# Optimization experiments

Hardware: AMD Instinct MI355X
Metric: run time of the kernel (lower is better)

## Reference

```python
import jax, jax.numpy as jnp
import numpy as np

NUM_HEADS = 16
ROPE_THETA = 10000.0


def setup_inputs() -> dict:
    key = jax.random.key(0)
    ks = jax.random.split(key, 5)
    B, S, D = 4, 2048, 2048
    scale = 0.02
    return {
        "x": jax.random.normal(ks[0], (B, S, D), dtype=jnp.float32),
        "wq": jax.random.normal(ks[1], (D, D), dtype=jnp.float32) * scale,
        "bq": jnp.zeros((D,), dtype=jnp.float32),
        "wk": jax.random.normal(ks[2], (D, D), dtype=jnp.float32) * scale,
        "bk": jnp.zeros((D,), dtype=jnp.float32),
        "wv": jax.random.normal(ks[3], (D, D), dtype=jnp.float32) * scale,
        "bv": jnp.zeros((D,), dtype=jnp.float32),
        "wo": jax.random.normal(ks[4], (D, D), dtype=jnp.float32) * scale,
        "bo": jnp.zeros((D,), dtype=jnp.float32),
    }


def _rotate_half(t):
    t1, t2 = jnp.split(t, 2, axis=-1)
    return jnp.concatenate([-t2, t1], axis=-1)


def _rope_cos_sin(seq_len, head_dim, dtype):
    inv_freq = 1.0 / (ROPE_THETA ** (jnp.arange(0, head_dim, 2, dtype=jnp.float32) / head_dim))
    freqs = jnp.einsum("s,d->sd", jnp.arange(seq_len, dtype=jnp.float32), inv_freq)
    emb = jnp.concatenate([freqs, freqs], axis=-1)  # [S, Dh]
    return jnp.cos(emb).astype(dtype)[None, None], jnp.sin(emb).astype(dtype)[None, None]


def reference(x, wq, bq, wk, bk, wv, bv, wo, bo):
    B, S, D = x.shape
    H = NUM_HEADS
    Dh = D // H

    def proj_heads(w, b):
        # [B,S,D] -> [B,H,S,Dh]
        return (x @ w.T + b).reshape(B, S, H, Dh).transpose(0, 2, 1, 3)

    q = proj_heads(wq, bq)
    k = proj_heads(wk, bk)
    v = proj_heads(wv, bv)

    cos, sin = _rope_cos_sin(S, Dh, x.dtype)
    q = q * cos + _rotate_half(q) * sin
    k = k * cos + _rotate_half(k) * sin

    # non-causal SDPA
    scores = jnp.einsum("bhsd,bhtd->bhst", q, k) / jnp.sqrt(jnp.asarray(Dh, x.dtype))
    attn = jax.nn.softmax(scores, axis=-1)
    ctx = jnp.einsum("bhst,bhtd->bhsd", attn, v)  # [B,H,S,Dh]

    ctx = ctx.transpose(0, 2, 1, 3).reshape(B, S, D)
    return ctx @ wo.T + bo
```

## Files before the change

kernel.cpp:

```cpp
#include <hip/hip_runtime.h>
#include <hip/hip_bf16.h>

typedef __bf16 bf16_t;
typedef __bf16 bf16x8 __attribute__((ext_vector_type(8)));
typedef float f32x4 __attribute__((ext_vector_type(4)));

#define MFMA16(A, B, C) __builtin_amdgcn_mfma_f32_16x16x32_bf16(A, B, C, 0, 0, 0)

#define GLOAD_LDS16(gp, lp)                                           \
    __builtin_amdgcn_global_load_lds(                                 \
        (const __attribute__((address_space(1))) void*)(gp),          \
        (__attribute__((address_space(3))) void*)(lp), 16, 0, 0)

__device__ __forceinline__ uint32_t pack2(bf16_t a, bf16_t b) {
    union { bf16_t h[2]; uint32_t u; } x;
    x.h[0] = a; x.h[1] = b;
    return x.u;
}

__global__ __launch_bounds__(256)
void cvt_f32_bf16(const float* __restrict__ src, bf16_t* __restrict__ dst, int n8)
{
    int stride = gridDim.x * 256;
    for (int i = blockIdx.x * 256 + threadIdx.x; i < n8; i += stride) {
        const float4 f0 = *(const float4*)(src + (size_t)i * 8);
        const float4 f1 = *(const float4*)(src + (size_t)i * 8 + 4);
        bf16x8 v = {(bf16_t)f0.x, (bf16_t)f0.y, (bf16_t)f0.z, (bf16_t)f0.w,
                    (bf16_t)f1.x, (bf16_t)f1.y, (bf16_t)f1.z, (bf16_t)f1.w};
        *(bf16x8*)(dst + (size_t)i * 8) = v;
    }
}

template <typename OT>
__global__ __launch_bounds__(256)
void gemm_bt_lds(const bf16_t* __restrict__ A, const bf16_t* __restrict__ W,
                 const float* __restrict__ bias, OT* __restrict__ C,
                 int M, int N, int K)
{
    __shared__ __align__(16) bf16_t lds_a[128 * 32];
    __shared__ __align__(16) bf16_t lds_b[128 * 32];

    const int tid  = threadIdx.x;
    const int wave = tid >> 6;
    const int lane = tid & 63;
    const int l15  = lane & 15;
    const int quad = lane >> 4;
    const int wm   = (wave >> 1) * 64;
    const int wn   = (wave & 1) * 64;

    const int bm = blockIdx.x * 128;
    const int bn = blockIdx.y * 128;

    const int srow = wave * 32 + (lane >> 2);
    const int scol = (lane & 3) * 8;

    const bf16_t* Ab = A + (size_t)(bm + srow) * K + scol;
    const bf16_t* Wb = W + (size_t)(bn + srow) * K + scol;
    bf16_t* la0 = &lds_a[wave * 32 * 32];
    bf16_t* lb0 = &lds_b[wave * 32 * 32];

    f32x4 acc[4][4] = {};

    for (int k0 = 0; k0 < K; k0 += 32) {
        GLOAD_LDS16(Ab + k0,          la0);
        GLOAD_LDS16(Ab + k0 + 16 * K, la0 + 16 * 32);
        GLOAD_LDS16(Wb + k0,          lb0);
        GLOAD_LDS16(Wb + k0 + 16 * K, lb0 + 16 * 32);
        __syncthreads();

        bf16x8 af[4], bfr[4];
        for (int i = 0; i < 4; ++i)
            af[i] = *(const bf16x8*)&lds_a[(wm + i * 16 + l15) * 32 + quad * 8];
        for (int j = 0; j < 4; ++j)
            bfr[j] = *(const bf16x8*)&lds_b[(wn + j * 16 + l15) * 32 + quad * 8];
        for (int i = 0; i < 4; ++i)
            for (int j = 0; j < 4; ++j)
                acc[i][j] = MFMA16(af[i], bfr[j], acc[i][j]);
        __syncthreads();
    }

    for (int i = 0; i < 4; ++i) {
        int mrow = bm + wm + i * 16 + quad * 4;
        for (int j = 0; j < 4; ++j) {
            int ncol = bn + wn + j * 16 + l15;
            float bval = bias[ncol];
            for (int r = 0; r < 4; ++r) {
                float v = acc[i][j][r] + bval;
                if constexpr (__is_same(OT, float))
                    C[(size_t)(mrow + r) * N + ncol] = v;
                else
                    C[(size_t)(mrow + r) * N + ncol] = (bf16_t)v;
            }
        }
    }
}

__global__ __launch_bounds__(256)
void rope_kernel(bf16_t* __restrict__ Q, bf16_t* __restrict__ Kk)
{
    size_t idx = (size_t)blockIdx.x * 256 + threadIdx.x;
    int j = (int)(idx & 63);
    size_t rest = idx >> 6;
    int h = (int)(rest & 15);
    size_t row = rest >> 4;
    int s = (int)(row & 2047);

    float inv = __expf(-(float)j * 0.14391156831212787f);
    float ang = (float)s * inv;
    float sn, cs;
    sincosf(ang, &sn, &cs);

    size_t base = row * 2048 + (size_t)h * 128 + j;
    float q0 = (float)Q[base], q1 = (float)Q[base + 64];
    Q[base]      = (bf16_t)(q0 * cs - q1 * sn);
    Q[base + 64] = (bf16_t)(q1 * cs + q0 * sn);
    float k0 = (float)Kk[base], k1 = (float)Kk[base + 64];
    Kk[base]      = (bf16_t)(k0 * cs - k1 * sn);
    Kk[base + 64] = (bf16_t)(k1 * cs + k0 * sn);
}

__global__ __launch_bounds__(256)
void transpose_v(const bf16_t* __restrict__ V, bf16_t* __restrict__ Vt)
{
    __shared__ __align__(16) bf16_t tile[64][72];
    int bh = blockIdx.z;
    int b = bh >> 4, h = bh & 15;
    int t0 = blockIdx.x * 64;
    int d0 = blockIdx.y * 64;
    int tid = threadIdx.x;

    for (int i = 0; i < 2; ++i) {
        int c = tid + i * 256;
        int row = c >> 3, col = (c & 7) * 8;
        *(uint4*)&tile[row][col] =
            *(const uint4*)&V[((size_t)(b * 2048 + t0 + row)) * 2048 + h * 128 + d0 + col];
    }
    __syncthreads();
    for (int i = 0; i < 2; ++i) {
        int c = tid + i * 256;
        int drow = c >> 3, tcol = (c & 7) * 8;
        __align__(16) bf16_t tmp[8];
        for (int j = 0; j < 8; ++j) tmp[j] = tile[tcol + j][drow];
        *(uint4*)&Vt[((size_t)((b * 16 + h) * 128 + d0 + drow)) * 2048 + t0 + tcol] =
            *(uint4*)tmp;
    }
}

__global__ __launch_bounds__(256, 2)
void flash_attn(const bf16_t* __restrict__ Q, const bf16_t* __restrict__ Kg,
                const bf16_t* __restrict__ Vt, bf16_t* __restrict__ Ctx)
{
    constexpr int S = 2048, H = 16, Dh = 128, D = 2048;
    constexpr int NT = S / 64;
    constexpr float scale = 0.08838834764831845f;

    __shared__ __align__(16) char smem[65536];
    bf16_t* qst = (bf16_t*)smem;

    const int bh = blockIdx.y;
    const int b = bh >> 4, h = bh & 15;
    const int q0 = blockIdx.x * 128;
    const int tid = threadIdx.x, wave = tid >> 6, lane = tid & 63;
    const int l15 = lane & 15, quad = lane >> 4;
    const int hi2 = quad >> 1;
    const int swz = (l15 & 7) << 4;

    const bf16_t* Qh  = Q  + ((size_t)b * S) * D + h * Dh;
    const bf16_t* Kh  = Kg + ((size_t)b * S) * D + h * Dh;
    const bf16_t* Vth = Vt + ((size_t)(b * H + h)) * Dh * S;

    int ks_off[4], vs_off[4];
#pragma unroll
    for (int i = 0; i < 4; ++i) {
        int kr = wave * 16 + i * 4 + (lane >> 4);
        int ksl = lane & 15;
        ks_off[i] = kr * D + ((ksl ^ (kr & 7)) * 8);
        int vr = wave * 32 + i * 8 + (lane >> 3);
        int vsl = lane & 7;
        vs_off[i] = vr * S + ((vsl ^ (vr & 7)) * 8);
    }

    for (int i = 0; i < 8; ++i) {
        int c = tid + i * 256;
        int row = c >> 4, col = (c & 15) * 8;
        *(uint4*)&qst[row * 136 + col] =
            *(const uint4*)&Qh[(size_t)(q0 + row) * D + col];
    }
    __syncthreads();
    bf16x8 aq[2][4];
    for (int g = 0; g < 2; ++g)
        for (int ks = 0; ks < 4; ++ks)
            aq[g][ks] = *(const bf16x8*)
                &qst[(wave * 32 + g * 16 + l15) * 136 + ks * 32 + quad * 8];
    __syncthreads();

    float m_i[2] = {-3.0e4f, -3.0e4f};
    float l_i[2] = {0.f, 0.f};
    f32x4 ot[2][8] = {};

    {
        char* kb = smem;
        char* vb = smem + 16384;
        const bf16_t* Vs = Vth;
#pragma unroll
        for (int i = 0; i < 4; ++i) {
            GLOAD_LDS16(Kh + ks_off[i], kb + wave * 4096 + i * 1024);
            GLOAD_LDS16(Vs + vs_off[i], vb + wave * 4096 + i * 1024);
        }
    }
    __syncthreads();

    for (int kt = 0; kt < NT; ++kt) {
        const int cur = kt & 1;
        if (kt + 1 < NT) {
            char* kb = smem + (cur ^ 1) * 32768;
            char* vb = kb + 16384;
            const bf16_t* Ks = Kh + (size_t)(kt + 1) * 64 * D;
            const bf16_t* Vs = Vth + (kt + 1) * 64;
#pragma unroll
            for (int i = 0; i < 4; ++i) {
                GLOAD_LDS16(Ks + ks_off[i], kb + wave * 4096 + i * 1024);
                GLOAD_LDS16(Vs + vs_off[i], vb + wave * 4096 + i * 1024);
            }
        }
        const char* k_raw  = smem + cur * 32768;
        const char* vt_raw = k_raw + 16384;

        f32x4 st[2][4] = {};
        __builtin_amdgcn_s_setprio(1);
        for (int ks = 0; ks < 4; ++ks)
            for (int kvs = 0; kvs < 4; ++kvs) {
                int row = kvs * 16 + l15;
                int off = (row * 256 + ks * 64 + quad * 16) ^ swz;
                bf16x8 kf = *(const bf16x8*)(k_raw + off);
                st[0][kvs] = MFMA16(kf, aq[0][ks], st[0][kvs]);
                st[1][kvs] = MFMA16(kf, aq[1][ks], st[1][kvs]);
            }
        __builtin_amdgcn_s_setprio(0);

        bf16x8 pb[2][2];
        for (int g = 0; g < 2; ++g) {
            float pm = -3.0e4f;
            for (int kvs = 0; kvs < 4; ++kvs)
                for (int r = 0; r < 4; ++r) pm = fmaxf(pm, st[g][kvs][r]);
            pm = fmaxf(pm, __shfl_xor(pm, 16));
            pm = fmaxf(pm, __shfl_xor(pm, 32));
            pm *= scale;

            if (!__all(pm - m_i[g] <= 8.0f)) {
                float mnew  = fmaxf(m_i[g], pm);
                float alpha = __expf(m_i[g] - mnew);
                for (int j = 0; j < 8; ++j) ot[g][j] *= alpha;
                l_i[g] *= alpha;
                m_i[g] = mnew;
            }

            uint32_t u[4][2];
            float ps = 0.f;
            for (int kvs = 0; kvs < 4; ++kvs) {
                bf16_t hq[4];
                for (int r = 0; r < 4; ++r) {
                    float pf = __expf(fmaf(st[g][kvs][r], scale, -m_i[g]));
                    hq[r] = (bf16_t)pf;
                    ps += (float)hq[r];
                }
                u[kvs][0] = pack2(hq[0], hq[1]);
                u[kvs][1] = pack2(hq[2], hq[3]);
            }
            ps += __shfl_xor(ps, 16);
            ps += __shfl_xor(ps, 32);
            l_i[g] += ps;

            int srcA = (quad & 1) * 32 + l15;
            int srcB = srcA + 16;
            for (int kk = 0; kk < 2; ++kk) {
                uint32_t a00 = __shfl((int)u[2 * kk + 0][0], srcA);
                uint32_t a01 = __shfl((int)u[2 * kk + 0][1], srcA);
                uint32_t a10 = __shfl((int)u[2 * kk + 1][0], srcA);
                uint32_t a11 = __shfl((int)u[2 * kk + 1][1], srcA);
                uint32_t b00 = __shfl((int)u[2 * kk + 0][0], srcB);
                uint32_t b01 = __shfl((int)u[2 * kk + 0][1], srcB);
                uint32_t b10 = __shfl((int)u[2 * kk + 1][0], srcB);
                uint32_t b11 = __shfl((int)u[2 * kk + 1][1], srcB);
                union { uint32_t w[4]; bf16x8 v; } cc;
                cc.w[0] = hi2 ? a10 : a00;
                cc.w[1] = hi2 ? a11 : a01;
                cc.w[2] = hi2 ? b10 : b00;
                cc.w[3] = hi2 ? b11 : b01;
                pb[g][kk] = cc.v;
            }
        }

        __builtin_amdgcn_s_setprio(1);
        for (int j = 0; j < 8; ++j)
            for (int kk = 0; kk < 2; ++kk) {
                int row = j * 16 + l15;
                int off = (row * 128 + kk * 64 + quad * 16) ^ swz;
                bf16x8 av = *(const bf16x8*)(vt_raw + off);
                ot[0][j] = MFMA16(av, pb[0][kk], ot[0][j]);
                ot[1][j] = MFMA16(av, pb[1][kk], ot[1][j]);
            }
        __builtin_amdgcn_s_setprio(0);

        __syncthreads();
    }

    for (int g = 0; g < 2; ++g) {
        float linv = 1.0f / l_i[g];
        size_t row = (size_t)b * S + q0 + wave * 32 + g * 16 + l15;
        for (int j = 0; j < 8; ++j) {
            union { bf16_t hh[4]; uint2 uu; } o;
            for (int r = 0; r < 4; ++r) o.hh[r] = (bf16_t)(ot[g][j][r] * linv);
            *(uint2*)&Ctx[row * D + h * Dh + j * 16 + quad * 4] = o.uu;
        }
    }
}

extern "C" void kernel_launch(void* const* d_in, const int* in_sizes, int n_in,
                              void* d_out, int out_size, void* d_ws, size_t ws_size,
                              hipStream_t stream)
{
    const float* x  = (const float*)d_in[0];
    const float* wq = (const float*)d_in[1];
    const float* bq = (const float*)d_in[2];
    const float* wk = (const float*)d_in[3];
    const float* bk = (const float*)d_in[4];
    const float* wv = (const float*)d_in[5];
    const float* bv = (const float*)d_in[6];
    const float* wo = (const float*)d_in[7];
    const float* bo = (const float*)d_in[8];
    float* out = (float*)d_out;

    const int B = 4, S = 2048, D = 2048, H = 16, Dh = 128;
    const int M = B * S;
    const size_t elems  = (size_t)M * D;
    const size_t welems = (size_t)D * D;

    bf16_t* Qw  = (bf16_t*)d_ws;
    bf16_t* Kw  = Qw + elems;
    bf16_t* Vw  = Kw + elems;
    bf16_t* Ctx = Vw;
    bf16_t* wob = Qw;

    bf16_t* outb = (bf16_t*)d_out;
    bf16_t* xb   = outb;
    bf16_t* wqb  = outb + elems;
    bf16_t* wkb  = wqb + welems;
    bf16_t* wvb  = wkb + welems;
    bf16_t* Vtw  = outb;

    cvt_f32_bf16<<<2048, 256, 0, stream>>>(x,  xb,  (int)(elems / 8));
    cvt_f32_bf16<<<2048, 256, 0, stream>>>(wq, wqb, (int)(welems / 8));
    cvt_f32_bf16<<<2048, 256, 0, stream>>>(wk, wkb, (int)(welems / 8));
    cvt_f32_bf16<<<2048, 256, 0, stream>>>(wv, wvb, (int)(welems / 8));

    dim3 gGemm(M / 128, D / 128);
    gemm_bt_lds<bf16_t><<<gGemm, 256, 0, stream>>>(xb, wqb, bq, Qw, M, D, D);
    gemm_bt_lds<bf16_t><<<gGemm, 256, 0, stream>>>(xb, wkb, bk, Kw, M, D, D);
    gemm_bt_lds<bf16_t><<<gGemm, 256, 0, stream>>>(xb, wvb, bv, Vw, M, D, D);

    size_t nrope = (size_t)M * H * 64;
    rope_kernel<<<(int)(nrope / 256), 256, 0, stream>>>(Qw, Kw);

    dim3 gT(S / 64, Dh / 64, B * H);
    transpose_v<<<gT, 256, 0, stream>>>(Vw, Vtw);

    dim3 gA(S / 128, B * H);
    flash_attn<<<gA, 256, 0, stream>>>(Qw, Kw, Vtw, Ctx);

    cvt_f32_bf16<<<2048, 256, 0, stream>>>(wo, wob, (int)(welems / 8));
    gemm_bt_lds<float><<<gGemm, 256, 0, stream>>>(Ctx, wob, bo, out, M, D, D);
}
```

Before: 791.7 us.

## Halve flash-attention KV tile to 32 and raise occupancy to four blocks per CU

Result: slower. 980.4 us (+23.8%).

```diff
diff --git a/kernel.cpp b/kernel.cpp
--- a/kernel.cpp
+++ b/kernel.cpp
@@ -146,15 +146,15 @@
     }
 }
 
-__global__ __launch_bounds__(256, 2)
+__global__ __launch_bounds__(256, 4)
 void flash_attn(const bf16_t* __restrict__ Q, const bf16_t* __restrict__ Kg,
                 const bf16_t* __restrict__ Vt, bf16_t* __restrict__ Ctx)
 {
     constexpr int S = 2048, H = 16, Dh = 128, D = 2048;
-    constexpr int NT = S / 64;
+    constexpr int NT = S / 32;
     constexpr float scale = 0.08838834764831845f;
 
-    __shared__ __align__(16) char smem[65536];
+    __shared__ __align__(16) char smem[34816];
     bf16_t* qst = (bf16_t*)smem;
 
     const int bh = blockIdx.y;
@@ -169,15 +169,13 @@
     const bf16_t* Kh  = Kg + ((size_t)b * S) * D + h * Dh;
     const bf16_t* Vth = Vt + ((size_t)(b * H + h)) * Dh * S;
 
-    int ks_off[4], vs_off[4];
+    int ks_off[2], vs_off[2];
 #pragma unroll
-    for (int i = 0; i < 4; ++i) {
-        int kr = wave * 16 + i * 4 + (lane >> 4);
-        int ksl = lane & 15;
-        ks_off[i] = kr * D + ((ksl ^ (kr & 7)) * 8);
-        int vr = wave * 32 + i * 8 + (lane >> 3);
-        int vsl = lane & 7;
-        vs_off[i] = vr * S + ((vsl ^ (vr & 7)) * 8);
+    for (int i = 0; i < 2; ++i) {
+        int kr = i * 16 + wave * 4 + (lane >> 4);
+        ks_off[i] = kr * D + (((lane & 15) ^ (kr & 7)) * 8);
+        int vr = i * 64 + wave * 16 + (lane >> 2);
+        vs_off[i] = vr * S + ((lane & 3) * 8);
     }
 
     for (int i = 0; i < 8; ++i) {
@@ -200,12 +198,11 @@
 
     {
         char* kb = smem;
-        char* vb = smem + 16384;
-        const bf16_t* Vs = Vth;
+        char* vb = smem + 8192;
 #pragma unroll
-        for (int i = 0; i < 4; ++i) {
-            GLOAD_LDS16(Kh + ks_off[i], kb + wave * 4096 + i * 1024);
-            GLOAD_LDS16(Vs + vs_off[i], vb + wave * 4096 + i * 1024);
+        for (int i = 0; i < 2; ++i) {
+            GLOAD_LDS16(Kh + ks_off[i],  kb + i * 4096 + wave * 1024);
+            GLOAD_LDS16(Vth + vs_off[i], vb + i * 4096 + wave * 1024);
         }
     }
     __syncthreads();
@@ -213,23 +210,23 @@
     for (int kt = 0; kt < NT; ++kt) {
         const int cur = kt & 1;
         if (kt + 1 < NT) {
-            char* kb = smem + (cur ^ 1) * 32768;
-            char* vb = kb + 16384;
-            const bf16_t* Ks = Kh + (size_t)(kt + 1) * 64 * D;
-            const bf16_t* Vs = Vth + (kt + 1) * 64;
+            char* kb = smem + (cur ^ 1) * 16384;
+            char* vb = kb + 8192;
+            const bf16_t* Ks = Kh + (size_t)(kt + 1) * 32 * D;
+            const bf16_t* Vs = Vth + (kt + 1) * 32;
 #pragma unroll
-            for (int i = 0; i < 4; ++i) {
-                GLOAD_LDS16(Ks + ks_off[i], kb + wave * 4096 + i * 1024);
-                GLOAD_LDS16(Vs + vs_off[i], vb + wave * 4096 + i * 1024);
-            }
-        }
-        const char* k_raw  = smem + cur * 32768;
-        const char* vt_raw = k_raw + 16384;
-
-        f32x4 st[2][4] = {};
+            for (int i = 0; i < 2; ++i) {
+                GLOAD_LDS16(Ks + ks_off[i], kb + i * 4096 + wave * 1024);
+                GLOAD_LDS16(Vs + vs_off[i], vb + i * 4096 + wave * 1024);
+            }
+        }
+        const char* k_raw  = smem + cur * 16384;
+        const char* vt_raw = k_raw + 8192;
+
+        f32x4 st[2][2] = {};
         __builtin_amdgcn_s_setprio(1);
         for (int ks = 0; ks < 4; ++ks)
-            for (int kvs = 0; kvs < 4; ++kvs) {
+            for (int kvs = 0; kvs < 2; ++kvs) {
                 int row = kvs * 16 + l15;
                 int off = (row * 256 + ks * 64 + quad * 16) ^ swz;
                 bf16x8 kf = *(const bf16x8*)(k_raw + off);
@@ -238,10 +235,10 @@
             }
         __builtin_amdgcn_s_setprio(0);
 
-        bf16x8 pb[2][2];
+        bf16x8 pb[2];
         for (int g = 0; g < 2; ++g) {
             float pm = -3.0e4f;
-            for (int kvs = 0; kvs < 4; ++kvs)
+            for (int kvs = 0; kvs < 2; ++kvs)
                 for (int r = 0; r < 4; ++r) pm = fmaxf(pm, st[g][kvs][r]);
             pm = fmaxf(pm, __shfl_xor(pm, 16));
             pm = fmaxf(pm, __shfl_xor(pm, 32));
@@ -255,9 +252,9 @@
                 m_i[g] = mnew;
             }
 
-            uint32_t u[4][2];
+            uint32_t u[2][2];
             float ps = 0.f;
-            for (int kvs = 0; kvs < 4; ++kvs) {
+            for (int kvs = 0; kvs < 2; ++kvs) {
                 bf16_t hq[4];
                 for (int r = 0; r < 4; ++r) {
                     float pf = __expf(fmaf(st[g][kvs][r], scale, -m_i[g]));
@@ -273,33 +270,29 @@
 
             int srcA = (quad & 1) * 32 + l15;
             int srcB = srcA + 16;
-            for (int kk = 0; kk < 2; ++kk) {
-                uint32_t a00 = __shfl((int)u[2 * kk + 0][0], srcA);
-                uint32_t a01 = __shfl((int)u[2 * kk + 0][1], srcA);
-                uint32_t a10 = __shfl((int)u[2 * kk + 1][0], srcA);
-                uint32_t a11 = __shfl((int)u[2 * kk + 1][1], srcA);
-                uint32_t b00 = __shfl((int)u[2 * kk + 0][0], srcB);
-                uint32_t b01 = __shfl((int)u[2 * kk + 0][1], srcB);
-                uint32_t b10 = __shfl((int)u[2 * kk + 1][0], srcB);
-                uint32_t b11 = __shfl((int)u[2 * kk + 1][1], srcB);
-                union { uint32_t w[4]; bf16x8 v; } cc;
-                cc.w[0] = hi2 ? a10 : a00;
-                cc.w[1] = hi2 ? a11 : a01;
-                cc.w[2] = hi2 ? b10 : b00;
-                cc.w[3] = hi2 ? b11 : b01;
-                pb[g][kk] = cc.v;
-            }
+            uint32_t a00 = __shfl((int)u[0][0], srcA);
+            uint32_t a01 = __shfl((int)u[0][1], srcA);
+            uint32_t a10 = __shfl((int)u[1][0], srcA);
+            uint32_t a11 = __shfl((int)u[1][1], srcA);
+            uint32_t b00 = __shfl((int)u[0][0], srcB);
+            uint32_t b01 = __shfl((int)u[0][1], srcB);
+            uint32_t b10 = __shfl((int)u[1][0], srcB);
+            uint32_t b11 = __shfl((int)u[1][1], srcB);
+            union { uint32_t w[4]; bf16x8 v; } cc;
+            cc.w[0] = hi2 ? a10 : a00;
+            cc.w[1] = hi2 ? a11 : a01;
+            cc.w[2] = hi2 ? b10 : b00;
+            cc.w[3] = hi2 ? b11 : b01;
+            pb[g] = cc.v;
         }
 
         __builtin_amdgcn_s_setprio(1);
-        for (int j = 0; j < 8; ++j)
-            for (int kk = 0; kk < 2; ++kk) {
-                int row = j * 16 + l15;
-                int off = (row * 128 + kk * 64 + quad * 16) ^ swz;
-                bf16x8 av = *(const bf16x8*)(vt_raw + off);
-                ot[0][j] = MFMA16(av, pb[0][kk], ot[0][j]);
-                ot[1][j] = MFMA16(av, pb[1][kk], ot[1][j]);
-            }
+        for (int j = 0; j < 8; ++j) {
+            int off = (j * 16 + l15) * 64 + quad * 16;
+            bf16x8 av = *(const bf16x8*)(vt_raw + off);
+            ot[0][j] = MFMA16(av, pb[0], ot[0][j]);
+            ot[1][j] = MFMA16(av, pb[1], ot[1][j]);
+        }
         __builtin_amdgcn_s_setprio(0);
 
         __syncthreads();
```
